# Performance work log

Hardware: AMD Instinct MI355X
Metric: run time of the kernel (lower is better)

The kernel has to match this reference:

```python
import jax, jax.numpy as jnp
import numpy as np
import math

RANKS = [16, 8, 4, 2, 1]          # generate_mrlora_ranks(32 // 2)
LORA_ALPHA = 16.0
SCALES = [LORA_ALPHA / math.sqrt(r) for r in RANKS]  # use_rslora=True
D_IN = 4096
D_OUT = 4096


def setup_inputs() -> dict:
    key = jax.random.key(0)
    ks = jax.random.split(key, 3 + 2 * len(RANKS))
    x = jax.random.normal(ks[0], (4, 2048, D_IN), dtype=jnp.float32)
    W = jax.random.normal(ks[1], (D_OUT, D_IN), dtype=jnp.float32) * (1.0 / math.sqrt(D_IN))
    b = jax.random.normal(ks[2], (D_OUT,), dtype=jnp.float32) * 0.01
    inp = {"x": x, "W": W, "b": b}
    for i, r in enumerate(RANKS):
        # A: [r, D_IN], B: [D_OUT, r] (torch nn.Linear weight layout)
        inp[f"A{r}"] = jax.random.normal(ks[3 + 2 * i], (r, D_IN), dtype=jnp.float32) * (1.0 / math.sqrt(D_IN))
        inp[f"B{r}"] = jax.random.normal(ks[4 + 2 * i], (D_OUT, r), dtype=jnp.float32) * 0.02
    inp["alphas"] = jnp.ones((len(RANKS),), dtype=jnp.float32)
    return inp


def reference(x, W, b, A16, B16, A8, B8, A4, B4, A2, B2, A1, B1, alphas):
    # base linear: x @ W.T + b
    out = jnp.einsum('bsd,od->bso', x, W) + b
    As = [A16, A8, A4, A2, A1]
    Bs = [B16, B8, B4, B2, B1]
    # dropout p=0 -> identity; per-rank low-rank update with learned + rslora scale
    for i, (A, B) in enumerate(zip(As, Bs)):
        coef = alphas[i] * SCALES[i]
        out = out + coef * jnp.einsum('bsr,or->bso', jnp.einsum('bsd,rd->bsr', x, A), B)
    return out
```

## Files before the change

kernel.cpp:

```cpp
#include <hip/hip_runtime.h>
#include <hip/hip_bf16.h>
#include <stdint.h>

#define DK 4096
#define MROWS 8192
#define NOUT 4096
#define KP 4160
#define KP_B (KP*2)
#define NT 65

typedef __attribute__((ext_vector_type(8))) __bf16 bf16x8;
typedef __attribute__((ext_vector_type(4))) float f32x4;
typedef unsigned short u16;

struct __align__(8) us4 { u16 x, y, z, w; };

__device__ __forceinline__ u16 f2bf(float f) {
  union { float f; uint32_t u; } v; v.f = f;
  uint32_t r = v.u + 0x7fffu + ((v.u >> 16) & 1u);
  return (u16)(r >> 16);
}

__device__ __forceinline__ void gload16(const void* g, void* l) {
  __builtin_amdgcn_global_load_lds(
      (const __attribute__((address_space(1))) unsigned int*)g,
      (__attribute__((address_space(3))) unsigned int*)l, 16, 0, 0);
}

__global__ void conv_x(const float* __restrict__ x, u16* __restrict__ xb) {
  int m = blockIdx.x, t = threadIdx.x;
  const float* src = x + (size_t)m * DK;
  u16* dst = xb + (size_t)m * KP;
#pragma unroll
  for (int j = 0; j < 4; ++j) {
    int col = (t + j * 256) * 4;
    float4 v = *reinterpret_cast<const float4*>(src + col);
    us4 o = { f2bf(v.x), f2bf(v.y), f2bf(v.z), f2bf(v.w) };
    *reinterpret_cast<us4*>(dst + col) = o;
  }
  if (t < 64) dst[4096 + t] = 0;
}

__global__ void build_W(const float* __restrict__ W,
                        const float* __restrict__ B16, const float* __restrict__ B8,
                        const float* __restrict__ B4,  const float* __restrict__ B2,
                        const float* __restrict__ B1,  const float* __restrict__ alphas,
                        u16* __restrict__ wb) {
  int n = blockIdx.x, t = threadIdx.x;
  const float* src = W + (size_t)n * DK;
  u16* dst = wb + (size_t)n * KP;
#pragma unroll
  for (int j = 0; j < 4; ++j) {
    int col = (t + j * 256) * 4;
    float4 v = *reinterpret_cast<const float4*>(src + col);
    us4 o = { f2bf(v.x), f2bf(v.y), f2bf(v.z), f2bf(v.w) };
    *reinterpret_cast<us4*>(dst + col) = o;
  }
  if (t < 64) {
    u16 val = 0;
    if (t < 31) {
      float coef; const float* Bp; int r, rl;
      if (t < 16)      { coef = alphas[0] * 4.0f;                Bp = B16; r = 16; rl = t; }
      else if (t < 24) { coef = alphas[1] * 5.656854249492381f;  Bp = B8;  r = 8;  rl = t - 16; }
      else if (t < 28) { coef = alphas[2] * 8.0f;                Bp = B4;  r = 4;  rl = t - 24; }
      else if (t < 30) { coef = alphas[3] * 11.313708498984761f; Bp = B2;  r = 2;  rl = t - 28; }
      else             { coef = alphas[4] * 16.0f;               Bp = B1;  r = 1;  rl = 0; }
      val = f2bf(coef * Bp[(size_t)n * r + rl]);
    }
    dst[4096 + t] = val;
  }
}

__global__ void build_A(const float* __restrict__ A16, const float* __restrict__ A8,
                        const float* __restrict__ A4,  const float* __restrict__ A2,
                        const float* __restrict__ A1,  u16* __restrict__ ab) {
  int rr = blockIdx.x, t = threadIdx.x;
  const float* src = nullptr;
  if (rr < 16)      src = A16 + (size_t)rr * DK;
  else if (rr < 24) src = A8 + (size_t)(rr - 16) * DK;
  else if (rr < 28) src = A4 + (size_t)(rr - 24) * DK;
  else if (rr < 30) src = A2 + (size_t)(rr - 28) * DK;
  else if (rr < 31) src = A1;
  u16* dst = ab + (size_t)rr * DK;
#pragma unroll
  for (int j = 0; j < 4; ++j) {
    int col = (t + j * 256) * 4;
    us4 o = { 0, 0, 0, 0 };
    if (src) {
      float4 v = *reinterpret_cast<const float4*>(src + col);
      o = { f2bf(v.x), f2bf(v.y), f2bf(v.z), f2bf(v.w) };
    }
    *reinterpret_cast<us4*>(dst + col) = o;
  }
}

__global__ __launch_bounds__(256, 2) void xa_gemm(u16* xb, const u16* __restrict__ ab) {
  __shared__ u16 Xs[64 * 64];
  __shared__ u16 Qs[32 * 64];
  int m0 = blockIdx.x * 64;
  int t = threadIdx.x, lane = t & 63, w = t >> 6;
  int l15 = lane & 15, lg = lane >> 4;
  f32x4 acc[2] = {};
  const char* xbase = (const char*)xb + (size_t)m0 * KP_B;
  for (int kt = 0; kt < 64; ++kt) {
    size_t kb = (size_t)kt * 128;
    __syncthreads();
#pragma unroll
    for (int i = 0; i < 2; ++i) {
      int chunk = w * 2 + i;
      int off = chunk * 1024 + lane * 16;
      int row = off >> 7, colB = off & 127;
      gload16(xbase + (size_t)row * KP_B + kb + colB, (char*)Xs + chunk * 1024);
    }
    {
      int off = w * 1024 + lane * 16;
      int row = off >> 7, colB = off & 127;
      gload16((const char*)ab + (size_t)row * (DK * 2) + kb + colB, (char*)Qs + w * 1024);
    }
    asm volatile("s_waitcnt vmcnt(0)" ::: "memory");
    __syncthreads();
#pragma unroll
    for (int ks = 0; ks < 2; ++ks) {
      bf16x8 xf = *reinterpret_cast<const bf16x8*>((const char*)Xs + (w * 16 + l15) * 128 + ks * 64 + lg * 16);
#pragma unroll
      for (int ni = 0; ni < 2; ++ni) {
        bf16x8 af = *reinterpret_cast<const bf16x8*>((const char*)Qs + (ni * 16 + l15) * 128 + ks * 64 + lg * 16);
        acc[ni] = __builtin_amdgcn_mfma_f32_16x16x32_bf16(xf, af, acc[ni], 0, 0, 0);
      }
    }
  }
#pragma unroll
  for (int ni = 0; ni < 2; ++ni)
#pragma unroll
    for (int r = 0; r < 4; ++r) {
      int m = m0 + w * 16 + lg * 4 + r;
      int c = 4096 + ni * 16 + l15;
      xb[(size_t)m * KP + c] = f2bf(acc[ni][r]);
    }
}

__device__ __forceinline__ void stage_tile(const char* gbase, char* lbase, int w, int lane, int i) {
  int chunk = (w << 2) + i;
  int row = (chunk << 3) + (lane >> 3);
  int src_c = ((lane & 7) ^ (lane >> 3)) << 4;
  gload16(gbase + (size_t)row * KP_B + src_c, lbase + chunk * 1024);
}

__device__ __forceinline__ bf16x8 rdfrag(const char* base, int row, int cb) {
  return *reinterpret_cast<const bf16x8*>(base + row * 128 + (cb ^ ((row & 7) << 4)));
}

__global__ __launch_bounds__(512, 2) void gemm_main(const u16* __restrict__ xb, const u16* __restrict__ wb,
                                                    const float* __restrict__ bias, float* __restrict__ out) {
  __shared__ u16 As0[256 * 64], As1[256 * 64];
  __shared__ u16 Bs0[256 * 64], Bs1[256 * 64];
  int bid = blockIdx.x;
  int swz = (bid & 7) * 64 + (bid >> 3);
  int mt = swz >> 4, nt = swz & 15;
  int m0 = mt * 256, n0 = nt * 256;
  int t = threadIdx.x, lane = t & 63, w = t >> 6;
  int wr = w >> 2, wc = w & 3;
  int l15 = lane & 15, lg = lane >> 4;

  f32x4 acc[8][4] = {};
  bf16x8 af[4][2], af2[4][2], bl[2][2], bh[2][2];

  const char* Ag = (const char*)xb + (size_t)m0 * KP_B;
  const char* Bg = (const char*)wb + (size_t)n0 * KP_B;
  char *AcA = (char*)As0, *AnA = (char*)As1, *AcB = (char*)Bs0, *AnB = (char*)Bs1;

#pragma unroll
  for (int i = 0; i < 4; ++i) stage_tile(Ag, AcA, w, lane, i);
#pragma unroll
  for (int i = 0; i < 4; ++i) stage_tile(Bg, AcB, w, lane, i);
  asm volatile("s_waitcnt vmcnt(0)" ::: "memory");
  __builtin_amdgcn_s_barrier();

  const int Arow = wr * 128 + l15;
  const int Brow = wc * 64 + l15;
  const int cb0 = lg * 16;

  for (int kt = 0; kt < NT; ++kt) {
    const char* Agk1 = Ag + (size_t)(kt + 1) * 128;
    const char* Bgk1 = Bg + (size_t)(kt + 1) * 128;
    const bool doS = (kt + 1 < NT);

#pragma unroll
    for (int mi = 0; mi < 4; ++mi)
#pragma unroll
      for (int ks = 0; ks < 2; ++ks)
        af[mi][ks] = rdfrag(AcA, Arow + mi * 16, cb0 + ks * 64);
#pragma unroll
    for (int ni = 0; ni < 2; ++ni)
#pragma unroll
      for (int ks = 0; ks < 2; ++ks)
        bl[ni][ks] = rdfrag(AcB, Brow + ni * 16, cb0 + ks * 64);
    if (doS) {
      stage_tile(Agk1, AnA, w, lane, 0); stage_tile(Agk1, AnA, w, lane, 1);
      stage_tile(Agk1, AnA, w, lane, 2); stage_tile(Agk1, AnA, w, lane, 3);
    }

#pragma unroll
    for (int ni = 0; ni < 2; ++ni)
#pragma unroll
      for (int ks = 0; ks < 2; ++ks)
        bh[ni][ks] = rdfrag(AcB, Brow + 32 + ni * 16, cb0 + ks * 64);
    if (doS) {
      stage_tile(Bgk1, AnB, w, lane, 0); stage_tile(Bgk1, AnB, w, lane, 1);
      stage_tile(Bgk1, AnB, w, lane, 2); stage_tile(Bgk1, AnB, w, lane, 3);
    }
    asm volatile("s_waitcnt lgkmcnt(4)" ::: "memory");
    __builtin_amdgcn_sched_barrier(0);
    __builtin_amdgcn_s_setprio(1);
#pragma unroll
    for (int mi = 0; mi < 4; ++mi)
#pragma unroll
      for (int ni = 0; ni < 2; ++ni)
#pragma unroll
        for (int ks = 0; ks < 2; ++ks)
          acc[mi][ni] = __builtin_amdgcn_mfma_f32_16x16x32_bf16(af[mi][ks], bl[ni][ks], acc[mi][ni], 0, 0, 0);
    __builtin_amdgcn_s_setprio(0);

#pragma unroll
    for (int mi = 0; mi < 4; ++mi)
#pragma unroll
      for (int ks = 0; ks < 2; ++ks)
        af2[mi][ks] = rdfrag(AcA, Arow + 64 + mi * 16, cb0 + ks * 64);
    asm volatile("s_waitcnt lgkmcnt(8)" ::: "memory");
    __builtin_amdgcn_sched_barrier(0);
    __builtin_amdgcn_s_setprio(1);
#pragma unroll
    for (int mi = 0; mi < 4; ++mi)
#pragma unroll
      for (int ni = 0; ni < 2; ++ni)
#pragma unroll
        for (int ks = 0; ks < 2; ++ks)
          acc[mi][ni + 2] = __builtin_amdgcn_mfma_f32_16x16x32_bf16(af[mi][ks], bh[ni][ks], acc[mi][ni + 2], 0, 0, 0);
    __builtin_amdgcn_s_setprio(0);

    asm volatile("s_waitcnt lgkmcnt(0)" ::: "memory");
    __builtin_amdgcn_sched_barrier(0);
    __builtin_amdgcn_s_setprio(1);
#pragma unroll
    for (int mi = 0; mi < 4; ++mi)
#pragma unroll
      for (int ni = 0; ni < 2; ++ni)
#pragma unroll
        for (int ks = 0; ks < 2; ++ks)
          acc[mi + 4][ni + 2] = __builtin_amdgcn_mfma_f32_16x16x32_bf16(af2[mi][ks], bh[ni][ks], acc[mi + 4][ni + 2], 0, 0, 0);
    __builtin_amdgcn_s_setprio(0);

    __builtin_amdgcn_s_setprio(1);
#pragma unroll
    for (int mi = 0; mi < 4; ++mi)
#pragma unroll
      for (int ni = 0; ni < 2; ++ni)
#pragma unroll
        for (int ks = 0; ks < 2; ++ks)
          acc[mi + 4][ni] = __builtin_amdgcn_mfma_f32_16x16x32_bf16(af2[mi][ks], bl[ni][ks], acc[mi + 4][ni], 0, 0, 0);
    __builtin_amdgcn_s_setprio(0);
    asm volatile("s_waitcnt vmcnt(0)" ::: "memory");
    __builtin_amdgcn_s_barrier();

    { char* tp = AcA; AcA = AnA; AnA = tp; }
    { char* tp = AcB; AcB = AnB; AnB = tp; }
  }

  float bn[4];
#pragma unroll
  for (int ni = 0; ni < 4; ++ni) bn[ni] = bias[n0 + wc * 64 + ni * 16 + l15];
#pragma unroll
  for (int mi = 0; mi < 8; ++mi) {
    int mbase = m0 + wr * 128 + mi * 16 + lg * 4;
#pragma unroll
    for (int ni = 0; ni < 4; ++ni) {
      int n = n0 + wc * 64 + ni * 16 + l15;
#pragma unroll
      for (int r = 0; r < 4; ++r)
        out[(size_t)(mbase + r) * NOUT + n] = acc[mi][ni][r] + bn[ni];
    }
  }
}

extern "C" void kernel_launch(void* const* d_in, const int* in_sizes, int n_in,
                              void* d_out, int out_size, void* d_ws, size_t ws_size,
                              hipStream_t stream) {
  const float* x   = (const float*)d_in[0];
  const float* W   = (const float*)d_in[1];
  const float* b   = (const float*)d_in[2];
  const float* A16 = (const float*)d_in[3];
  const float* B16 = (const float*)d_in[4];
  const float* A8  = (const float*)d_in[5];
  const float* B8  = (const float*)d_in[6];
  const float* A4  = (const float*)d_in[7];
  const float* B4  = (const float*)d_in[8];
  const float* A2  = (const float*)d_in[9];
  const float* B2  = (const float*)d_in[10];
  const float* A1  = (const float*)d_in[11];
  const float* B1  = (const float*)d_in[12];
  const float* alphas = (const float*)d_in[13];

  char* ws = (char*)d_ws;
  u16* xb = (u16*)ws;
  u16* wb = (u16*)(ws + 68157440);
  u16* ab = (u16*)(ws + 68157440 + 34078720);
  float* out = (float*)d_out;

  conv_x<<<MROWS, 256, 0, stream>>>(x, xb);
  build_W<<<NOUT, 256, 0, stream>>>(W, B16, B8, B4, B2, B1, alphas, wb);
  build_A<<<32, 256, 0, stream>>>(A16, A8, A4, A2, A1, ab);
  xa_gemm<<<MROWS / 64, 256, 0, stream>>>(xb, ab);
  gemm_main<<<(MROWS / 256) * (NOUT / 256), 512, 0, stream>>>(xb, wb, b, out);
}
```

Baseline: 316.3 us.

## Fuse x bf16 conversion with low-rank x·A projection in one kernel

Merges the fp32-to-bf16 conversion of x with the x·A LoRA projection, so x is read once in fp32 and A-products are computed straight from registers. This removes a separate pass that re-read the bf16 x copy from global memory. Each block handles 16 rows with four waves splitting the K dimension, then reduces the partial sums through shared memory. Padding columns 4128..4159 are zeroed explicitly. The tradeoff is that A fragments are loaded uncached from global memory by every block, and the work is split into small blocks.

```diff
diff --git a/kernel.cpp b/kernel.cpp
--- a/kernel.cpp
+++ b/kernel.cpp
@@ -25,20 +25,6 @@
   __builtin_amdgcn_global_load_lds(
       (const __attribute__((address_space(1))) unsigned int*)g,
       (__attribute__((address_space(3))) unsigned int*)l, 16, 0, 0);
-}
-
-__global__ void conv_x(const float* __restrict__ x, u16* __restrict__ xb) {
-  int m = blockIdx.x, t = threadIdx.x;
-  const float* src = x + (size_t)m * DK;
-  u16* dst = xb + (size_t)m * KP;
-#pragma unroll
-  for (int j = 0; j < 4; ++j) {
-    int col = (t + j * 256) * 4;
-    float4 v = *reinterpret_cast<const float4*>(src + col);
-    us4 o = { f2bf(v.x), f2bf(v.y), f2bf(v.z), f2bf(v.w) };
-    *reinterpret_cast<us4*>(dst + col) = o;
-  }
-  if (t < 64) dst[4096 + t] = 0;
 }
 
 __global__ void build_W(const float* __restrict__ W,
@@ -94,49 +80,51 @@
   }
 }
 
-__global__ __launch_bounds__(256, 2) void xa_gemm(u16* xb, const u16* __restrict__ ab) {
-  __shared__ u16 Xs[64 * 64];
-  __shared__ u16 Qs[32 * 64];
-  int m0 = blockIdx.x * 64;
+__global__ __launch_bounds__(256, 2) void conv_xa(const float* __restrict__ x, u16* __restrict__ xb,
+                                                  const u16* __restrict__ ab) {
+  __shared__ float part[4][2][64][4];
+  int m0 = blockIdx.x * 16;
   int t = threadIdx.x, lane = t & 63, w = t >> 6;
   int l15 = lane & 15, lg = lane >> 4;
-  f32x4 acc[2] = {};
-  const char* xbase = (const char*)xb + (size_t)m0 * KP_B;
-  for (int kt = 0; kt < 64; ++kt) {
-    size_t kb = (size_t)kt * 128;
-    __syncthreads();
-#pragma unroll
-    for (int i = 0; i < 2; ++i) {
-      int chunk = w * 2 + i;
-      int off = chunk * 1024 + lane * 16;
-      int row = off >> 7, colB = off & 127;
-      gload16(xbase + (size_t)row * KP_B + kb + colB, (char*)Xs + chunk * 1024);
-    }
-    {
-      int off = w * 1024 + lane * 16;
-      int row = off >> 7, colB = off & 127;
-      gload16((const char*)ab + (size_t)row * (DK * 2) + kb + colB, (char*)Qs + w * 1024);
-    }
-    asm volatile("s_waitcnt vmcnt(0)" ::: "memory");
-    __syncthreads();
-#pragma unroll
-    for (int ks = 0; ks < 2; ++ks) {
-      bf16x8 xf = *reinterpret_cast<const bf16x8*>((const char*)Xs + (w * 16 + l15) * 128 + ks * 64 + lg * 16);
-#pragma unroll
-      for (int ni = 0; ni < 2; ++ni) {
-        bf16x8 af = *reinterpret_cast<const bf16x8*>((const char*)Qs + (ni * 16 + l15) * 128 + ks * 64 + lg * 16);
-        acc[ni] = __builtin_amdgcn_mfma_f32_16x16x32_bf16(xf, af, acc[ni], 0, 0, 0);
-      }
-    }
-  }
-#pragma unroll
-  for (int ni = 0; ni < 2; ++ni)
-#pragma unroll
-    for (int r = 0; r < 4; ++r) {
-      int m = m0 + w * 16 + lg * 4 + r;
-      int c = 4096 + ni * 16 + l15;
-      xb[(size_t)m * KP + c] = f2bf(acc[ni][r]);
-    }
+  int row = m0 + l15;
+  const float* xp = x + (size_t)row * DK + w * 1024 + lg * 8;
+  u16* xbp = xb + (size_t)row * KP + w * 1024 + lg * 8;
+  const u16* a0 = ab + (size_t)l15 * DK + w * 1024 + lg * 8;
+  const u16* a1 = ab + (size_t)(16 + l15) * DK + w * 1024 + lg * 8;
+  f32x4 acc0 = {}, acc1 = {};
+  union { bf16x8 v; us4 h[2]; } xf;
+#pragma unroll 4
+  for (int kk = 0; kk < 32; ++kk) {
+    float4 v0 = *reinterpret_cast<const float4*>(xp + kk * 32);
+    float4 v1 = *reinterpret_cast<const float4*>(xp + kk * 32 + 4);
+    xf.h[0] = us4{ f2bf(v0.x), f2bf(v0.y), f2bf(v0.z), f2bf(v0.w) };
+    xf.h[1] = us4{ f2bf(v1.x), f2bf(v1.y), f2bf(v1.z), f2bf(v1.w) };
+    *reinterpret_cast<us4*>(xbp + kk * 32) = xf.h[0];
+    *reinterpret_cast<us4*>(xbp + kk * 32 + 4) = xf.h[1];
+    bf16x8 af0 = *reinterpret_cast<const bf16x8*>(a0 + kk * 32);
+    bf16x8 af1 = *reinterpret_cast<const bf16x8*>(a1 + kk * 32);
+    acc0 = __builtin_amdgcn_mfma_f32_16x16x32_bf16(xf.v, af0, acc0, 0, 0, 0);
+    acc1 = __builtin_amdgcn_mfma_f32_16x16x32_bf16(xf.v, af1, acc1, 0, 0, 0);
+  }
+  *reinterpret_cast<f32x4*>(&part[w][0][lane][0]) = acc0;
+  *reinterpret_cast<f32x4*>(&part[w][1][lane][0]) = acc1;
+  __syncthreads();
+  if (w == 0) {
+#pragma unroll
+    for (int ni = 0; ni < 2; ++ni) {
+      f32x4 s = *reinterpret_cast<const f32x4*>(&part[0][ni][lane][0]);
+#pragma unroll
+      for (int ww = 1; ww < 4; ++ww)
+        s += *reinterpret_cast<const f32x4*>(&part[ww][ni][lane][0]);
+#pragma unroll
+      for (int r = 0; r < 4; ++r)
+        xb[(size_t)(m0 + lg * 4 + r) * KP + 4096 + ni * 16 + l15] = f2bf(s[r]);
+    }
+  }
+  if (t < 128) {
+    us4 z = { 0, 0, 0, 0 };
+    *reinterpret_cast<us4*>(xb + (size_t)(m0 + (t >> 3)) * KP + 4128 + (t & 7) * 4) = z;
+  }
 }
 
 __device__ __forceinline__ void stage_tile(const char* gbase, char* lbase, int w, int lane, int i) {
@@ -306,9 +294,8 @@
   u16* ab = (u16*)(ws + 68157440 + 34078720);
   float* out = (float*)d_out;
 
-  conv_x<<<MROWS, 256, 0, stream>>>(x, xb);
+  build_A<<<32, 256, 0, stream>>>(A16, A8, A4, A2, A1, ab);
+  conv_xa<<<MROWS / 16, 256, 0, stream>>>(x, xb, ab);
   build_W<<<NOUT, 256, 0, stream>>>(W, B16, B8, B4, B2, B1, alphas, wb);
-  build_A<<<32, 256, 0, stream>>>(A16, A8, A4, A2, A1, ab);
-  xa_gemm<<<MROWS / 64, 256, 0, stream>>>(xb, ab);
   gemm_main<<<(MROWS / 256) * (NOUT / 256), 512, 0, stream>>>(xb, wb, b, out);
 }
```

New measurement: 293.7 us (median of 2 runs). 7.1% less time.
